# Kernel optimization log

Hardware: AMD Instinct MI355X
Metric: run time of the kernel (lower is better)

The kernel has to match this reference:

```python
import jax, jax.numpy as jnp
import numpy as np

N_HEAD, D_K, D_V = 8, 64, 64
TOPK = 16
B, N_R, N_W = 256, 64, 64
D_READ = D_WRITE = D_OUT = 512
TEMP = float(np.power(D_K, 0.5))
EPS = 1e-7  # 10e-8 in original Sparse_attention


def sparse_attention(a, top_k):
    # a: (rows, n); RIMs Sparse_attention: threshold at k-th largest, clamp, renormalize
    if a.shape[-1] <= top_k:
        return a
    delta = jax.lax.top_k(a, top_k)[0][..., -1:] + EPS
    w = jnp.clip(a - delta, 0.0, None)
    return w / (jnp.sum(w, axis=-1, keepdims=True) + EPS)


def setup_inputs() -> dict:
    key = jax.random.key(0)
    ks = jax.random.split(key, 8)
    q = jax.random.normal(ks[0], (B, N_R, D_READ), dtype=jnp.float32)
    k = jax.random.normal(ks[1], (B, N_W, D_WRITE), dtype=jnp.float32)
    v = jax.random.normal(ks[2], (B, N_W, D_WRITE), dtype=jnp.float32)
    # GroupLinearLayer weights: (num_blocks, d_in, n_head*d)
    Wq = 0.02 * jax.random.normal(ks[3], (N_R, D_READ, N_HEAD * D_K), dtype=jnp.float32)
    Wk = 0.02 * jax.random.normal(ks[4], (N_W, D_WRITE, N_HEAD * D_K), dtype=jnp.float32)
    Wv = 0.02 * jax.random.normal(ks[5], (N_W, D_WRITE, N_HEAD * D_V), dtype=jnp.float32)
    fc_w = 0.02 * jax.random.normal(ks[6], (D_OUT, N_HEAD * D_V), dtype=jnp.float32)
    fc_b = jnp.zeros((D_OUT,), dtype=jnp.float32)
    gate_w = 0.02 * jax.random.normal(ks[7], (D_OUT, N_HEAD * D_V), dtype=jnp.float32)
    gate_b = jnp.zeros((D_OUT,), dtype=jnp.float32)
    return {"q": q, "k": k, "v": v, "Wq": Wq, "Wk": Wk, "Wv": Wv,
            "fc_w": fc_w, "fc_b": fc_b, "gate_w": gate_w, "gate_b": gate_b}


def reference(q, k, v, Wq, Wk, Wv, fc_w, fc_b, gate_w, gate_b):
    # grouped per-block projections: out[b,n] = x[b,n] @ W[n]
    qp = jnp.einsum('bnd,nde->bne', q, Wq).reshape(B, N_R, N_HEAD, D_K)
    kp = jnp.einsum('bnd,nde->bne', k, Wk).reshape(B, N_W, N_HEAD, D_K)
    vp = jnp.einsum('bnd,nde->bne', v, Wv).reshape(B, N_W, N_HEAD, D_V)
    # (H*B, len, d) with head-major leading dim, matching permute(2,0,1,3).view(-1,...)
    qh = qp.transpose(2, 0, 1, 3).reshape(N_HEAD * B, N_R, D_K)
    kh = kp.transpose(2, 0, 1, 3).reshape(N_HEAD * B, N_W, D_K)
    vh = vp.transpose(2, 0, 1, 3).reshape(N_HEAD * B, N_W, D_V)
    scores = jnp.einsum('ijk,ilk->ijl', qh, kh) / TEMP          # (HB, Nr, Nw)
    a = jnp.exp(jnp.max(scores, axis=-1, keepdims=True))        # (HB, Nr, 1)
    # flag=True: softmax over the query-block dim (permute/softmax/reshape)
    a = jax.nn.softmax(a[..., 0], axis=-1)                      # (HB, Nr)
    a = sparse_attention(a, TOPK)                               # (HB, Nr)
    attn = a[..., None]                                         # (HB, Nr, 1)
    # einsum 'ijk,ikl->ijl' with attn's k-dim == 1 broadcasts: attn * sum_k v
    out = attn * jnp.sum(vh, axis=1, keepdims=True)             # (HB, Nr, Dv)
    out = out.reshape(N_HEAD, B, N_R, D_V).transpose(1, 2, 0, 3).reshape(B, N_R, N_HEAD * D_V)
    fc_out = out @ fc_w.T + fc_b
    gate = jax.nn.sigmoid(out @ gate_w.T + gate_b)
    output = gate * jnp.tanh(fc_out)                            # residual=True gating
    return output
```

## Files before the change

kernel.cpp:

```cpp
#include <hip/hip_runtime.h>
#include <stdint.h>

#define B_    256
#define NR    64
#define NW    64
#define DIN   512
#define NH    8
#define DK    64
#define E_    512
#define TEMP_INV 0.125f
#define EPSV  1e-7f

typedef unsigned short u16;
typedef unsigned int   u32;
typedef _Float16 f16;
typedef __attribute__((ext_vector_type(2))) float    floatx2;
typedef __attribute__((ext_vector_type(4))) float    floatx4;
typedef __attribute__((ext_vector_type(4))) u32      uintx4;
typedef __attribute__((ext_vector_type(2))) _Float16 halfx2;
typedef __attribute__((ext_vector_type(8))) _Float16 halfx8;

__device__ __forceinline__ halfx2 h2(u32 u) { union { u32 u; halfx2 h; } c; c.u = u; return c.h; }
__device__ __forceinline__ u32 pkh(float a, float b) {
    union { halfx2 h; u32 u; } c; c.h = (halfx2){(f16)a, (f16)b}; return c.u;
}


#define STORE_A(sbuf) do {                                                    \
        u32 hh_[8];                                                           \
        _Pragma("unroll")                                                     \
        for (int c = 0; c < 4; c++) {                                         \
            hh_[2*c]   = pkh(pa[c].x, pa[c].y);                               \
            hh_[2*c+1] = pkh(pa[c].z, pa[c].w);                               \
        }                                                                     \
        *(uintx4*)&As[sbuf][(2*ahalf+0)*1024 + arow*8] =                      \
            (uintx4){hh_[0],hh_[1],hh_[2],hh_[3]};                            \
        *(uintx4*)&As[sbuf][(2*ahalf+1)*1024 + arow*8] =                      \
            (uintx4){hh_[4],hh_[5],hh_[6],hh_[7]};                            \
    } while (0)

#define STORE_B(sbuf, pb) do {                                                \
        _Pragma("unroll")                                                     \
        for (int eo = 0; eo < 2; eo++) {                                      \
            uintx4 hv_ = (uintx4){pkh(pb[0][eo], pb[1][eo]),                  \
                                  pkh(pb[2][eo], pb[3][eo]),                  \
                                  pkh(pb[4][eo], pb[5][eo]),                  \
                                  pkh(pb[6][eo], pb[7][eo])};                 \
            *(uintx4*)&Bs[sbuf][kq*1024 + eo*512 + p*8] = hv_;                \
        }                                                                     \
    } while (0)

#define LOAD_A(kn) do {                                                       \
        _Pragma("unroll")                                                     \
        for (int c = 0; c < 4; c++)                                           \
            pa[c] = *(const floatx4*)(aptr + (kn) + c * 4);                   \
    } while (0)

#define LOAD_B(pb, kn) do {                                                   \
        _Pragma("unroll")                                                     \
        for (int j = 0; j < 8; j++)                                           \
            pb[j] = *(const floatx2*)(wptr + (size_t)((kn) + kq*8 + j) * E_); \
    } while (0)

#define COMPUTE(sbuf) do {                                                    \
        halfx8 af_[4], bf_[4];                                                \
        _Pragma("unroll")                                                     \
        for (int mi = 0; mi < 4; mi++)                                        \
            af_[mi] = *(const halfx8*)&As[sbuf][quad*1024 + (wm + mi*16 + l15)*8]; \
        _Pragma("unroll")                                                     \
        for (int ni = 0; ni < 4; ni++) {                                      \
            int e_ = wn + ni*16 + l15;                                        \
            bf_[ni] = *(const halfx8*)&Bs[sbuf][quad*1024 + (e_&1)*512 + (e_>>1)*8]; \
        }                                                                     \
        _Pragma("unroll")                                                     \
        for (int mi = 0; mi < 4; mi++)                                        \
            _Pragma("unroll")                                                 \
            for (int ni = 0; ni < 4; ni++)                                    \
                acc[mi][ni] = __builtin_amdgcn_mfma_f32_16x16x32_f16(         \
                    af_[mi], bf_[ni], acc[mi][ni], 0, 0, 0);                  \
    } while (0)

#define PHASE_BARRIER() do {                                                  \
        asm volatile("s_waitcnt lgkmcnt(0)" ::: "memory");                    \
        __builtin_amdgcn_s_barrier();                                         \
        __builtin_amdgcn_sched_barrier(0);                                    \
    } while (0)

__global__ __launch_bounds__(256)
void proj_kernel(const float* __restrict__ q, const float* __restrict__ kk_,
                 const float* __restrict__ v,
                 const float* __restrict__ Wq, const float* __restrict__ Wk,
                 const float* __restrict__ Wv,
                 f16* __restrict__ qp, f16* __restrict__ kp,
                 f16* __restrict__ vp, float* __restrict__ vsum)
{
    const float* X; const float* W; f16* dst;
    if (blockIdx.z == 0)      { X = q;   W = Wq; dst = qp; }
    else if (blockIdx.z == 1) { X = kk_; W = Wk; dst = kp; }
    else                      { X = v;   W = Wv; dst = vp; }

    const int n  = blockIdx.x * 8 + (blockIdx.y & 7);
    const int t_ = blockIdx.y >> 3;
    const int m0 = (t_ >> 2) * 128;
    const int n0 = (t_ & 3) * 128;

    __shared__ u16 As[2][4096];
    __shared__ u16 Bs[2][4096];

    const int tid  = threadIdx.x;
    const int lane = tid & 63;
    const int wave = tid >> 6;
    const int wm   = (wave >> 1) * 64;
    const int wn   = (wave & 1) * 64;
    const int l15  = lane & 15;
    const int quad = lane >> 4;

    floatx4 acc[4][4];
#pragma unroll
    for (int i = 0; i < 4; i++)
#pragma unroll
        for (int j = 0; j < 4; j++) acc[i][j] = (floatx4){0.f, 0.f, 0.f, 0.f};

    const int arow  = tid >> 1;
    const int ahalf = tid & 1;
    const float* aptr = X + ((size_t)(m0 + arow) * NW + n) * DIN + ahalf * 16;
    const int kq = tid >> 6;
    const int p  = tid & 63;
    const float* wptr = W + (size_t)n * (DIN * E_) + n0 + 2 * p;

    floatx4 pa[4];
    floatx2 pb0[8], pb1[8];

    LOAD_A(0);
    LOAD_B(pb0, 0);
    LOAD_B(pb1, 32);

#pragma unroll 1
    for (int it2 = 0; it2 < 8; it2++) {
        const int k0 = it2 * 64;
        STORE_A(0);
        STORE_B(0, pb0);
        LOAD_A(k0 + 32);
        if (it2 < 7) { LOAD_B(pb0, k0 + 64); }
        PHASE_BARRIER();
        COMPUTE(0);
        STORE_A(1);
        STORE_B(1, pb1);
        if (it2 < 7) { LOAD_A(k0 + 64); LOAD_B(pb1, k0 + 96); }
        PHASE_BARRIER();
        COMPUTE(1);
    }

    if (dst) {
#pragma unroll
        for (int mi = 0; mi < 4; mi++) {
            int rowb = m0 + wm + mi * 16 + quad * 4;
#pragma unroll
            for (int ni = 0; ni < 4; ni++) {
                int col = n0 + wn + ni * 16 + l15;
#pragma unroll
                for (int r = 0; r < 4; r++)
                    dst[((size_t)(rowb + r) * NW + n) * E_ + col] = (f16)acc[mi][ni][r];
            }
        }
    } else {
#pragma unroll
        for (int mi = 0; mi < 4; mi++) {
            int rowb = m0 + wm + mi * 16 + quad * 4;
#pragma unroll
            for (int ni = 0; ni < 4; ni++) {
                int col = n0 + wn + ni * 16 + l15;
#pragma unroll
                for (int r = 0; r < 4; r++)
                    atomicAdd(&vsum[(size_t)(rowb + r) * E_ + col], acc[mi][ni][r]);
            }
        }
    }
}

__global__ __launch_bounds__(256)
void vsum_kernel(const f16* __restrict__ vp, float* __restrict__ vsum)
{
    const int b = blockIdx.x;
    const int t = threadIdx.x;
    const u32* src = (const u32*)vp + (size_t)b * NW * (E_ / 2) + t;
    float s0 = 0.f, s1 = 0.f;
#pragma unroll 4
    for (int nn = 0; nn < NW; nn++) {
        halfx2 hv = h2(src[(size_t)nn * (E_ / 2)]);
        s0 += (float)hv.x;
        s1 += (float)hv.y;
    }
    *(floatx2*)&vsum[(size_t)b * E_ + 2 * t] = (floatx2){s0, s1};
}

__global__ __launch_bounds__(256)
void attn_kernel(const f16* __restrict__ qp, const f16* __restrict__ kp,
                 float* __restrict__ attnT)
{
    const int h = blockIdx.x >> 8;
    const int b = blockIdx.x & 255;
    __shared__ u16 qs[64 * 72];
    __shared__ u16 ks[64 * 72];
    __shared__ float ms[64];

    const int t    = threadIdx.x;
    const int w    = t >> 6;
    const int lane = t & 63;
    const int l15  = lane & 15;
    const int quad = lane >> 4;

    {
        const int r = t >> 2, c = t & 3;
        const f16* qsrc = qp + ((size_t)(b * NR + r)) * E_ + h * DK + c * 16;
        const f16* ksrc = kp + ((size_t)(b * NW + r)) * E_ + h * DK + c * 16;
        *(uintx4*)&qs[r * 72 + c * 16]     = *(const uintx4*)(qsrc);
        *(uintx4*)&qs[r * 72 + c * 16 + 8] = *(const uintx4*)(qsrc + 8);
        *(uintx4*)&ks[r * 72 + c * 16]     = *(const uintx4*)(ksrc);
        *(uintx4*)&ks[r * 72 + c * 16 + 8] = *(const uintx4*)(ksrc + 8);
    }
    __syncthreads();

    floatx4 sc[4];
#pragma unroll
    for (int ni = 0; ni < 4; ni++) sc[ni] = (floatx4){0.f, 0.f, 0.f, 0.f};

    halfx8 af[2];
#pragma unroll
    for (int kk = 0; kk < 2; kk++)
        af[kk] = *(const halfx8*)&qs[(w * 16 + l15) * 72 + kk * 32 + quad * 8];
#pragma unroll
    for (int ni = 0; ni < 4; ni++)
#pragma unroll
        for (int kk = 0; kk < 2; kk++) {
            halfx8 bf = *(const halfx8*)&ks[(ni * 16 + l15) * 72 + kk * 32 + quad * 8];
            sc[ni] = __builtin_amdgcn_mfma_f32_16x16x32_f16(af[kk], bf, sc[ni], 0, 0, 0);
        }

#pragma unroll
    for (int r = 0; r < 4; r++) {
        float rm = fmaxf(fmaxf(sc[0][r], sc[1][r]), fmaxf(sc[2][r], sc[3][r]));
#pragma unroll
        for (int d = 1; d < 16; d <<= 1) rm = fmaxf(rm, __shfl_xor(rm, d));
        if (l15 == 0) ms[w * 16 + quad * 4 + r] = rm;
    }
    __syncthreads();

    if (t < 64) {
        float mm = ms[lane] * TEMP_INV;
        float e = expf(mm);
        float mx = e;
#pragma unroll
        for (int d = 1; d < 64; d <<= 1) mx = fmaxf(mx, __shfl_xor(mx, d));
        float tt = expf(e - mx);
        float S = tt;
#pragma unroll
        for (int d = 1; d < 64; d <<= 1) S += __shfl_xor(S, d);
        float s = tt / S;

        float cur = s, v16 = 0.f;
        for (int itk = 0; itk < 16; itk++) {
            float mv = cur;
#pragma unroll
            for (int d = 1; d < 64; d <<= 1) mv = fmaxf(mv, __shfl_xor(mv, d));
            unsigned long long bal = __ballot(cur == mv);
            int first = __ffsll(bal) - 1;
            if (lane == first) cur = -1e30f;
            v16 = mv;
        }
        float delta = v16 + EPSV;
        float ww = fmaxf(s - delta, 0.f);
        float sw = ww;
#pragma unroll
        for (int d = 1; d < 64; d <<= 1) sw += __shfl_xor(sw, d);
        attnT[((size_t)b * NR + lane) * NH + h] = ww / (sw + EPSV);
    }
}

__global__ __launch_bounds__(256)
void fcv_kernel(const float* __restrict__ vsum, const float* __restrict__ fc_w,
                const float* __restrict__ gate_w, float* __restrict__ fcv,
                float* __restrict__ gatev)
{
    const int ohalf = blockIdx.x >> 3;
    const int bq    = blockIdx.x & 7;
    const int h     = blockIdx.y;
    const float* W  = blockIdx.z ? gate_w : fc_w;
    float* out      = blockIdx.z ? gatev : fcv;
    const int o     = ohalf * 256 + threadIdx.x;

    __shared__ float vs[32 * 64];
#pragma unroll
    for (int i = 0; i < 8; i++) {
        int idx = i * 256 + threadIdx.x;
        int bb = idx >> 6, d = idx & 63;
        vs[idx] = vsum[(size_t)(bq * 32 + bb) * E_ + h * DK + d];
    }
    floatx4 wr[16];
#pragma unroll
    for (int c = 0; c < 16; c++)
        wr[c] = *(const floatx4*)(W + (size_t)o * E_ + h * DK + c * 4);
    __syncthreads();

    for (int bb = 0; bb < 32; bb++) {
        const floatx4* vr = (const floatx4*)&vs[bb * 64];
        float a = 0.f;
#pragma unroll
        for (int c = 0; c < 16; c++) {
            floatx4 vv = vr[c];
            a += vv.x * wr[c].x + vv.y * wr[c].y + vv.z * wr[c].z + vv.w * wr[c].w;
        }
        out[((size_t)(bq * 32 + bb) * NH + h) * E_ + o] = a;
    }
}

__global__ __launch_bounds__(256)
void final_kernel(const float* __restrict__ fcv, const float* __restrict__ gatev,
                  const float* __restrict__ attnT, const float* __restrict__ fc_b,
                  const float* __restrict__ gate_b, float* __restrict__ out)
{
    const int b   = blockIdx.x;
    const int r0  = blockIdx.y * 16;
    const int tid = threadIdx.x;
    __shared__ float ats[16 * NH];

    if (tid < 16 * NH) ats[tid] = attnT[(size_t)b * NR * NH + r0 * NH + tid];

    float fr[2][8], gr[2][8];
#pragma unroll
    for (int half = 0; half < 2; half++) {
        int o = half * 256 + tid;
#pragma unroll
        for (int hh = 0; hh < 8; hh++) {
            fr[half][hh] = fcv[((size_t)b * NH + hh) * E_ + o];
            gr[half][hh] = gatev[((size_t)b * NH + hh) * E_ + o];
        }
    }
    float bfc0 = fc_b[tid],   bfc1 = fc_b[256 + tid];
    float bgt0 = gate_b[tid], bgt1 = gate_b[256 + tid];
    __syncthreads();

    for (int r = 0; r < 16; r++) {
        float a[8];
#pragma unroll
        for (int hh = 0; hh < 8; hh++) a[hh] = ats[r * NH + hh];
#pragma unroll
        for (int half = 0; half < 2; half++) {
            int o = half * 256 + tid;
            float fc = half ? bfc1 : bfc0;
            float gt = half ? bgt1 : bgt0;
#pragma unroll
            for (int hh = 0; hh < 8; hh++) {
                fc = fmaf(a[hh], fr[half][hh], fc);
                gt = fmaf(a[hh], gr[half][hh], gt);
            }
            float g  = 1.f / (1.f + __expf(-gt));
            float e2 = __expf(2.f * fc);
            float th = 1.f - 2.f / (e2 + 1.f);
            out[((size_t)(b * NR + r0 + r)) * E_ + o] = g * th;
        }
    }
}

extern "C" void kernel_launch(void* const* d_in, const int* in_sizes, int n_in,
                              void* d_out, int out_size, void* d_ws, size_t ws_size,
                              hipStream_t stream)
{
    const float* q      = (const float*)d_in[0];
    const float* k      = (const float*)d_in[1];
    const float* v      = (const float*)d_in[2];
    const float* Wq     = (const float*)d_in[3];
    const float* Wk     = (const float*)d_in[4];
    const float* Wv     = (const float*)d_in[5];
    const float* fc_w   = (const float*)d_in[6];
    const float* fc_b   = (const float*)d_in[7];
    const float* gate_w = (const float*)d_in[8];
    const float* gate_b = (const float*)d_in[9];
    float* out = (float*)d_out;

    char* ws = (char*)d_ws;
    f16* qp = (f16*)(ws);
    f16* kp = (f16*)(ws + (16u << 20));

    const bool big = ws_size >= (50u << 20);
    f16* vp; float* vsum; float* attnT; float* fcv; float* gatev;
    if (big) {
        vp    = (f16*)(ws + (32u << 20));
        vsum  = (float*)(ws + (48u << 20));
        attnT = (float*)(ws + (48u << 20) + 524288);
        fcv   = (float*)(ws + (32u << 20));
        gatev = (float*)(ws + (36u << 20));
    } else {
        vp    = nullptr;
        vsum  = (float*)(ws + 33554432);
        attnT = (float*)(ws + 33554432 + 524288);
        fcv   = (float*)(ws + 33554432 + 2 * 524288);
        gatev = (float*)(ws + 33554432 + 2 * 524288 + 4194304);
        hipMemsetAsync(vsum, 0, 524288, stream);
    }

    hipLaunchKernelGGL(proj_kernel, dim3(8, 64, 3), dim3(256), 0, stream,
                       q, k, v, Wq, Wk, Wv, qp, kp, vp, vsum);
    hipLaunchKernelGGL(attn_kernel, dim3(2048), dim3(256), 0, stream, qp, kp, attnT);
    if (big)
        hipLaunchKernelGGL(vsum_kernel, dim3(256), dim3(256), 0, stream, vp, vsum);
    hipLaunchKernelGGL(fcv_kernel, dim3(16, 8, 2), dim3(256), 0, stream,
                       vsum, fc_w, gate_w, fcv, gatev);
    hipLaunchKernelGGL(final_kernel, dim3(256, 4), dim3(256), 0, stream,
                       fcv, gatev, attnT, fc_b, gate_b, out);
}
```

Baseline: 355.5 us.

## Shrink projection GEMM M-tile to 64 and raise occupancy with launch bounds

Halves the proj_kernel tile from 128x128 to 64x128 rows per block, doubling the grid, and adds a min-blocks-per-CU launch bound of 4. It also drops one prefetch register buffer for B and reorders the loads so a single buffer is reused across both LDS stages. The goal is more resident blocks and better latency hiding in the grouped projection GEMM. The cost is that each W tile is read twice as often and there is less MFMA work per LDS load.

```diff
diff --git a/kernel.cpp b/kernel.cpp
--- a/kernel.cpp
+++ b/kernel.cpp
@@ -27,16 +27,9 @@
 
 
 #define STORE_A(sbuf) do {                                                    \
-        u32 hh_[8];                                                           \
-        _Pragma("unroll")                                                     \
-        for (int c = 0; c < 4; c++) {                                         \
-            hh_[2*c]   = pkh(pa[c].x, pa[c].y);                               \
-            hh_[2*c+1] = pkh(pa[c].z, pa[c].w);                               \
-        }                                                                     \
-        *(uintx4*)&As[sbuf][(2*ahalf+0)*1024 + arow*8] =                      \
-            (uintx4){hh_[0],hh_[1],hh_[2],hh_[3]};                            \
-        *(uintx4*)&As[sbuf][(2*ahalf+1)*1024 + arow*8] =                      \
-            (uintx4){hh_[4],hh_[5],hh_[6],hh_[7]};                            \
+        uintx4 ha_ = (uintx4){pkh(pa[0].x, pa[0].y), pkh(pa[0].z, pa[0].w),   \
+                              pkh(pa[1].x, pa[1].y), pkh(pa[1].z, pa[1].w)};  \
+        *(uintx4*)&As[sbuf][kq8 * 512 + arow * 8] = ha_;                      \
     } while (0)
 
 #define STORE_B(sbuf, pb) do {                                                \
@@ -46,14 +39,13 @@
                                   pkh(pb[2][eo], pb[3][eo]),                  \
                                   pkh(pb[4][eo], pb[5][eo]),                  \
                                   pkh(pb[6][eo], pb[7][eo])};                 \
-            *(uintx4*)&Bs[sbuf][kq*1024 + eo*512 + p*8] = hv_;                \
+            *(uintx4*)&Bs[sbuf][kq * 1024 + eo * 512 + p * 8] = hv_;          \
         }                                                                     \
     } while (0)
 
 #define LOAD_A(kn) do {                                                       \
-        _Pragma("unroll")                                                     \
-        for (int c = 0; c < 4; c++)                                           \
-            pa[c] = *(const floatx4*)(aptr + (kn) + c * 4);                   \
+        pa[0] = *(const floatx4*)(aptr + (kn));                               \
+        pa[1] = *(const floatx4*)(aptr + (kn) + 4);                           \
     } while (0)
 
 #define LOAD_B(pb, kn) do {                                                   \
@@ -63,17 +55,17 @@
     } while (0)
 
 #define COMPUTE(sbuf) do {                                                    \
-        halfx8 af_[4], bf_[4];                                                \
+        halfx8 af_[2], bf_[4];                                                \
         _Pragma("unroll")                                                     \
-        for (int mi = 0; mi < 4; mi++)                                        \
-            af_[mi] = *(const halfx8*)&As[sbuf][quad*1024 + (wm + mi*16 + l15)*8]; \
+        for (int mi = 0; mi < 2; mi++)                                        \
+            af_[mi] = *(const halfx8*)&As[sbuf][quad*512 + (wm + mi*16 + l15)*8]; \
         _Pragma("unroll")                                                     \
         for (int ni = 0; ni < 4; ni++) {                                      \
             int e_ = wn + ni*16 + l15;                                        \
             bf_[ni] = *(const halfx8*)&Bs[sbuf][quad*1024 + (e_&1)*512 + (e_>>1)*8]; \
         }                                                                     \
         _Pragma("unroll")                                                     \
-        for (int mi = 0; mi < 4; mi++)                                        \
+        for (int mi = 0; mi < 2; mi++)                                        \
             _Pragma("unroll")                                                 \
             for (int ni = 0; ni < 4; ni++)                                    \
                 acc[mi][ni] = __builtin_amdgcn_mfma_f32_16x16x32_f16(         \
@@ -86,7 +78,7 @@
         __builtin_amdgcn_sched_barrier(0);                                    \
     } while (0)
 
-__global__ __launch_bounds__(256)
+__global__ __launch_bounds__(256, 4)
 void proj_kernel(const float* __restrict__ q, const float* __restrict__ kk_,
                  const float* __restrict__ v,
                  const float* __restrict__ Wq, const float* __restrict__ Wk,
@@ -99,61 +91,59 @@
     else if (blockIdx.z == 1) { X = kk_; W = Wk; dst = kp; }
     else                      { X = v;   W = Wv; dst = vp; }
 
-    const int n  = blockIdx.x * 8 + (blockIdx.y & 7);
-    const int t_ = blockIdx.y >> 3;
-    const int m0 = (t_ >> 2) * 128;
-    const int n0 = (t_ & 3) * 128;
-
-    __shared__ u16 As[2][4096];
+    const int n  = blockIdx.x * 8 + ((blockIdx.y >> 2) & 7);
+    const int m0 = (blockIdx.y & 3) * 64;
+    const int n0 = (blockIdx.y >> 5) * 128;
+
+    __shared__ u16 As[2][2048];
     __shared__ u16 Bs[2][4096];
 
     const int tid  = threadIdx.x;
     const int lane = tid & 63;
     const int wave = tid >> 6;
-    const int wm   = (wave >> 1) * 64;
+    const int wm   = (wave >> 1) * 32;
     const int wn   = (wave & 1) * 64;
     const int l15  = lane & 15;
     const int quad = lane >> 4;
 
-    floatx4 acc[4][4];
-#pragma unroll
-    for (int i = 0; i < 4; i++)
+    floatx4 acc[2][4];
+#pragma unroll
+    for (int i = 0; i < 2; i++)
 #pragma unroll
         for (int j = 0; j < 4; j++) acc[i][j] = (floatx4){0.f, 0.f, 0.f, 0.f};
 
-    const int arow  = tid >> 1;
-    const int ahalf = tid & 1;
-    const float* aptr = X + ((size_t)(m0 + arow) * NW + n) * DIN + ahalf * 16;
+    const int arow = tid >> 2;
+    const int kq8  = tid & 3;
+    const float* aptr = X + ((size_t)(m0 + arow) * NW + n) * DIN + kq8 * 8;
     const int kq = tid >> 6;
     const int p  = tid & 63;
     const float* wptr = W + (size_t)n * (DIN * E_) + n0 + 2 * p;
 
-    floatx4 pa[4];
-    floatx2 pb0[8], pb1[8];
+    floatx4 pa[2];
+    floatx2 pb[8];
 
     LOAD_A(0);
-    LOAD_B(pb0, 0);
-    LOAD_B(pb1, 32);
+    LOAD_B(pb, 0);
 
 #pragma unroll 1
     for (int it2 = 0; it2 < 8; it2++) {
         const int k0 = it2 * 64;
         STORE_A(0);
-        STORE_B(0, pb0);
+        STORE_B(0, pb);
         LOAD_A(k0 + 32);
-        if (it2 < 7) { LOAD_B(pb0, k0 + 64); }
+        LOAD_B(pb, k0 + 32);
         PHASE_BARRIER();
         COMPUTE(0);
         STORE_A(1);
-        STORE_B(1, pb1);
-        if (it2 < 7) { LOAD_A(k0 + 64); LOAD_B(pb1, k0 + 96); }
+        STORE_B(1, pb);
+        if (it2 < 7) { LOAD_A(k0 + 64); LOAD_B(pb, k0 + 64); }
         PHASE_BARRIER();
         COMPUTE(1);
     }
 
     if (dst) {
 #pragma unroll
-        for (int mi = 0; mi < 4; mi++) {
+        for (int mi = 0; mi < 2; mi++) {
             int rowb = m0 + wm + mi * 16 + quad * 4;
 #pragma unroll
             for (int ni = 0; ni < 4; ni++) {
@@ -165,7 +155,7 @@
         }
     } else {
 #pragma unroll
-        for (int mi = 0; mi < 4; mi++) {
+        for (int mi = 0; mi < 2; mi++) {
             int rowb = m0 + wm + mi * 16 + quad * 4;
 #pragma unroll
             for (int ni = 0; ni < 4; ni++) {
@@ -399,7 +389,7 @@
         hipMemsetAsync(vsum, 0, 524288, stream);
     }
 
-    hipLaunchKernelGGL(proj_kernel, dim3(8, 64, 3), dim3(256), 0, stream,
+    hipLaunchKernelGGL(proj_kernel, dim3(8, 128, 3), dim3(256), 0, stream,
                        q, k, v, Wq, Wk, Wv, qp, kp, vp, vsum);
     hipLaunchKernelGGL(attn_kernel, dim3(2048), dim3(256), 0, stream, qp, kp, attnT);
     if (big)
```

Result: slower. 374.5 us (+5.3%).
